# Optimization experiments

Measured on AMD Instinct MI355X. Metric: run time of the kernel, lower is better.

The kernel has to match this reference:

```python
import jax, jax.numpy as jnp
import numpy as np
import math

B, S, DIM = 2, 4096, 1024
H, HD = 16, 64            # n_heads, head_dim
BLK, TOPK = 512, 3        # moba_block_size, moba_topk
NEG_INF = -10000.0


def setup_inputs() -> dict:
    key = jax.random.key(0)
    ks = jax.random.split(key, 5)
    scale = 1.0 / math.sqrt(DIM)
    x = jax.random.normal(ks[0], (B, S, DIM), dtype=jnp.float32)
    wq = jax.random.normal(ks[1], (DIM, DIM), dtype=jnp.float32) * scale
    wk = jax.random.normal(ks[2], (DIM, DIM), dtype=jnp.float32) * scale
    wv = jax.random.normal(ks[3], (DIM, DIM), dtype=jnp.float32) * scale
    wo = jax.random.normal(ks[4], (DIM, DIM), dtype=jnp.float32) * scale
    # rotary tables over half of head_dim
    inv_freq = 1.0 / (10000.0 ** (jnp.arange(0, HD, 2, dtype=jnp.float32) / HD))
    ang = jnp.arange(S, dtype=jnp.float32)[:, None] * inv_freq[None, :]  # [S, HD//2]
    return {"x": x, "wq": wq, "wk": wk, "wv": wv, "wo": wo,
            "cos": jnp.cos(ang), "sin": jnp.sin(ang)}


def _rotate(t, cos, sin):
    # t: [B, H, S, HD]; rotate-half rotary embedding
    c = cos[None, None, :, :]
    s = sin[None, None, :, :]
    t1, t2 = jnp.split(t, 2, axis=-1)
    return jnp.concatenate([t1 * c - t2 * s, t1 * s + t2 * c], axis=-1)


def _moba_forward(x, wq, wk, wv, wo, cos, sin):
    bs, seq_len, dim = x.shape
    inv_sqrt_d = 1.0 / math.sqrt(HD)
    q = (x @ wq).reshape(bs, seq_len, H, HD).transpose(0, 2, 1, 3)  # [B,H,S,D]
    k = (x @ wk).reshape(bs, seq_len, H, HD).transpose(0, 2, 1, 3)
    v = (x @ wv).reshape(bs, seq_len, H, HD).transpose(0, 2, 1, 3)
    q = _rotate(q, cos, sin)
    k = _rotate(k, cos, sin)

    nb = seq_len // BLK  # num_blocks (S divisible by BLK -> pad_len = 0)
    k_blocks = k.reshape(bs, H, nb, BLK, HD)
    v_blocks = v.reshape(bs, H, nb, BLK, HD)

    # gating: q against block means, with block-causal mask
    block_repr = k_blocks.mean(axis=3)  # [B,H,nb,D]
    gating = jnp.einsum('bhsd,bhnd->bhsn', q, block_repr) * inv_sqrt_d
    q_block = jnp.arange(seq_len) // BLK
    future = q_block[:, None] < jnp.arange(nb)[None, :]  # [S, nb]
    gating = jnp.where(future[None, None], NEG_INF, gating)
    _, sel = jax.lax.top_k(gating, TOPK)  # [B,H,S,TOPK]

    # one chunk per block of queries; chunk uses indices of its middle query
    nc = seq_len // BLK
    mids = jnp.arange(nc) * BLK + BLK // 2
    chunk_sel = sel[:, :, mids, :]  # [B,H,nc,TOPK]

    idx = chunk_sel.reshape(bs, H, nc * TOPK)[..., None, None]  # [B,H,nc*k,1,1]
    k_sel = jnp.take_along_axis(k_blocks, idx, axis=2).reshape(bs, H, nc, TOPK * BLK, HD)
    v_sel = jnp.take_along_axis(v_blocks, idx, axis=2).reshape(bs, H, nc, TOPK * BLK, HD)

    q_ch = q.reshape(bs, H, nc, BLK, HD)
    scores = jnp.einsum('bhcqd,bhckd->bhcqk', q_ch, k_sel) * inv_sqrt_d
    probs = jax.nn.softmax(scores.astype(jnp.float32), axis=-1).astype(scores.dtype)
    out = jnp.einsum('bhcqk,bhckd->bhcqd', probs, v_sel)  # [B,H,nc,BLK,D]
    out = out.reshape(bs, H, seq_len, HD).transpose(0, 2, 1, 3).reshape(bs, seq_len, dim)
    return out @ wo


def reference(x, wq, wk, wv, wo, cos, sin):
    return _moba_forward(x, wq, wk, wv, wo, cos, sin)
```

## Files before the change

### kernel.cpp

```cpp
#include <hip/hip_runtime.h>

typedef short bf16x8 __attribute__((ext_vector_type(8)));
typedef float f32x4 __attribute__((ext_vector_type(4)));
typedef float f32x16 __attribute__((ext_vector_type(16)));

#define AS1 __attribute__((address_space(1)))
#define AS3 __attribute__((address_space(3)))
#define GLOAD16(g, l) __builtin_amdgcn_global_load_lds((const AS1 unsigned int*)(g), (AS3 unsigned int*)(l), 16, 0, 0)

#define B_   2
#define S_   4096
#define DIM_ 1024
#define H_   16
#define HD_  64
#define BLK_ 512
#define SCLQ 0.18033688011112042f

static __device__ __forceinline__ unsigned short f2bf(float x){
  unsigned int u = __builtin_bit_cast(unsigned int, x);
  u += 0x7fffu + ((u >> 16) & 1u);
  return (unsigned short)(u >> 16);
}

static __device__ __forceinline__ unsigned cvtpk(float lo, float hi){
  unsigned r;
  asm("v_cvt_pk_bf16_f32 %0, %1, %2" : "=v"(r) : "v"(lo), "v"(hi));
  return r;
}
static __device__ __forceinline__ void plswap(unsigned &a, unsigned &b){
  asm("v_permlane32_swap_b32 %0, %1" : "+v"(a), "+v"(b));
}
static __device__ __forceinline__ bf16x8 mkpa(unsigned a, unsigned b, unsigned c, unsigned d){
  int4 v = make_int4((int)a,(int)b,(int)c,(int)d);
  return __builtin_bit_cast(bf16x8, v);
}

__global__ __launch_bounds__(256) void k_convert_x(const float4* __restrict__ x, ushort4* __restrict__ xb){
  int i = blockIdx.x * 256 + threadIdx.x;
  float4 v = x[i];
  xb[i] = make_ushort4(f2bf(v.x), f2bf(v.y), f2bf(v.z), f2bf(v.w));
}

__global__ __launch_bounds__(256) void k_transpose_w(
    const float* __restrict__ w0, const float* __restrict__ w1,
    const float* __restrict__ w2, const float* __restrict__ w3,
    unsigned short* __restrict__ wqkvT, unsigned short* __restrict__ woT){
  __shared__ float tl[32][33];
  int z = blockIdx.z;
  const float* w = z==0 ? w0 : z==1 ? w1 : z==2 ? w2 : w3;
  unsigned short* t = (z==3) ? woT : (wqkvT + (size_t)z*1024*1024);
  int nb = blockIdx.x*32, kb = blockIdx.y*32;
  int tx = threadIdx.x & 31, ty = threadIdx.x >> 5;
  #pragma unroll
  for(int i=0;i<4;i++) tl[ty+8*i][tx] = w[(size_t)(kb+ty+8*i)*DIM_ + nb+tx];
  __syncthreads();
  #pragma unroll
  for(int i=0;i<4;i++) t[(size_t)(nb+ty+8*i)*DIM_ + kb+tx] = f2bf(tl[tx][ty+8*i]);
}

__global__ __launch_bounds__(256) void k_prepw(const float* __restrict__ cosT, const float* __restrict__ sinT,
                                               float* __restrict__ W){
  int idx = blockIdx.x*256 + threadIdx.x;
  int s = idx >> 6, j = idx & 63;
  W[idx] = (j < 32) ? cosT[s*32 + j] : sinT[s*32 + j - 32];
}

__global__ __launch_bounds__(256) void k_xp(const float* __restrict__ x, const float* __restrict__ W,
                                            float* __restrict__ Xp2){
  __shared__ float Xl[16*128];
  __shared__ float Wl[16*64];
  int bid = blockIdx.x;
  int dt = bid & 7, ss = (bid>>3)&1, n = (bid>>4)&7, b = bid>>7;
  int tid = threadIdx.x;
  int jt = tid & 15, dtl = tid >> 4;
  int dbase = dt*128;
  int s0 = n*512 + ss*256;
  f32x4 acc[8];
  #pragma unroll
  for(int i=0;i<8;i++) acc[i] = (f32x4){0.f,0.f,0.f,0.f};

  for(int ch=0; ch<16; ch++){
    int sb = s0 + ch*16;
    #pragma unroll
    for(int i=0;i<2;i++){
      int g = i*256 + tid;
      int row = g>>5, col = g&31;
      GLOAD16(x + ((size_t)b*S_ + sb + row)*DIM_ + dbase + col*4, (char*)Xl + g*16);
    }
    {
      int row = tid>>4, col = tid&15;
      GLOAD16(W + (size_t)(sb + row)*64 + col*4, (char*)Wl + tid*16);
    }
    __syncthreads();
    #pragma unroll
    for(int s=0;s<16;s++){
      f32x4 wv = *(const f32x4*)&Wl[s*64 + jt*4];
      f32x4 x0 = *(const f32x4*)&Xl[s*128 + dtl*8];
      f32x4 x1 = *(const f32x4*)&Xl[s*128 + dtl*8 + 4];
      #pragma unroll
      for(int dd=0;dd<4;dd++) acc[dd]   += wv * x0[dd];
      #pragma unroll
      for(int dd=0;dd<4;dd++) acc[dd+4] += wv * x1[dd];
    }
    __syncthreads();
  }
  size_t base = ((size_t)(ss*16 + b*8 + n))*1024;
  #pragma unroll
  for(int dd=0;dd<8;dd++){
    size_t row = base + dbase + dtl*8 + dd;
    *(f32x4*)&Xp2[row*64 + jt*4] = acc[dd];
  }
}

__global__ __launch_bounds__(256) void k_bsum(const float* __restrict__ Xp2, const float* __restrict__ wk,
                                              float* __restrict__ bsum){
  __shared__ float red[4][64];
  int bid = blockIdx.x;
  int h = bid & 15, n = (bid>>4)&7, b = bid>>7;
  int tid = threadIdx.x;
  int jj = tid & 63, dgrp = tid >> 6;
  int j = jj & 31;
  size_t r0 = ((size_t)(b*8 + n))*1024;
  size_t r1 = ((size_t)(16 + b*8 + n))*1024;
  float acc = 0.0f;
  for(int i=0;i<256;i++){
    int d = dgrp*256 + i;
    float xc = Xp2[(r0 + d)*64 + j]      + Xp2[(r1 + d)*64 + j];
    float xs = Xp2[(r0 + d)*64 + 32 + j] + Xp2[(r1 + d)*64 + 32 + j];
    float u = wk[(size_t)d*1024 + h*64 + j];
    float v = wk[(size_t)d*1024 + h*64 + 32 + j];
    acc += (jj < 32) ? (xc*u - xs*v) : (xs*u + xc*v);
  }
  red[dgrp][jj] = acc;
  __syncthreads();
  if(tid < 64){
    float s = red[0][tid] + red[1][tid] + red[2][tid] + red[3][tid];
    bsum[(((size_t)(b*16+h))*8 + n)*64 + tid] = s;
  }
}

__global__ __launch_bounds__(256) void k_qmid(const float* __restrict__ x, const float* __restrict__ wq,
                                              float* __restrict__ qpart){
  __shared__ float xr[128];
  int bid = blockIdx.x;
  int ks  = blockIdx.y;
  int b = bid >> 3, c = bid & 7;
  int mid = c*BLK_ + BLK_/2;
  int tid = threadIdx.x;
  if(tid < 128) xr[tid] = x[((size_t)b*S_ + mid)*DIM_ + ks*128 + tid];
  __syncthreads();
  float acc[4] = {0,0,0,0};
  for(int k=0;k<128;k++){
    float xv = xr[k];
    #pragma unroll
    for(int i=0;i<4;i++) acc[i] += xv * wq[(size_t)(ks*128+k)*1024 + i*256 + tid];
  }
  #pragma unroll
  for(int i=0;i<4;i++) qpart[((size_t)ks*16 + bid)*1024 + i*256 + tid] = acc[i];
}

__global__ __launch_bounds__(256) void k_sel(const float* __restrict__ qpart, const float* __restrict__ bsum,
                                             const float* __restrict__ cosT, const float* __restrict__ sinT,
                                             int* __restrict__ sel){
  int bid = blockIdx.x;
  int b = bid >> 3, c = bid & 7;
  int mid = c*BLK_ + BLK_/2;
  int tid = threadIdx.x;
  int hg = tid >> 4, ln = tid & 15;
  size_t qb0 = (size_t)bid*1024 + hg*64;
  auto qsum = [&](int idx){
    float s = 0.0f;
    #pragma unroll
    for(int ks=0;ks<8;ks++) s += qpart[(size_t)ks*16384 + qb0 + idx];
    return s;
  };
  float rv[4];
  #pragma unroll
  for(int i=0;i<4;i++){
    int jj = ln*4 + i; int j = jj & 31;
    float q1 = qsum(j), q2 = qsum(32+j);
    float c0 = cosT[(size_t)mid*32 + j], s0 = sinT[(size_t)mid*32 + j];
    rv[i] = (jj < 32) ? (q1*c0 - q2*s0) : (q1*s0 + q2*c0);
  }
  float g[8];
  #pragma unroll
  for(int n=0;n<8;n++){
    const float* bs = bsum + (((size_t)(b*16+hg))*8 + n)*64 + ln*4;
    float p = rv[0]*bs[0] + rv[1]*bs[1] + rv[2]*bs[2] + rv[3]*bs[3];
    p += __shfl_xor(p,1); p += __shfl_xor(p,2); p += __shfl_xor(p,4); p += __shfl_xor(p,8);
    g[n] = p * (1.0f/512.0f) * 0.125f;
  }
  if(ln == 0){
    for(int n=c+1;n<8;n++) g[n] = -10000.0f;
    int base = ((b*16+hg)*8 + c)*3;
    #pragma unroll
    for(int t=0;t<3;t++){
      int bi = 0; float bv = g[0];
      for(int n=1;n<8;n++) if(g[n] > bv){ bv = g[n]; bi = n; }
      sel[base + t] = bi;
      g[bi] = -3.4e38f;
    }
  }
}

template<int MODE>
__global__ __launch_bounds__(512, 2) void k_gemmq(const unsigned short* __restrict__ A,
                                                  const unsigned short* __restrict__ Bt,
                                                  unsigned short* __restrict__ dq, unsigned short* __restrict__ dk,
                                                  unsigned short* __restrict__ dv, float* __restrict__ dstf,
                                                  const float* __restrict__ cosT, const float* __restrict__ sinT,
                                                  int M, int N, int K){
  __shared__ unsigned short lA[2][128*64];
  __shared__ unsigned short lB[2][128*64];
  int bm = blockIdx.y*128, bn = blockIdx.x*128;
  int tid = threadIdx.x, w = tid>>6, lane = tid&63;
  int wr = w>>1, wc = w&1;
  int l15 = lane&15, lh = lane>>4;
  f32x4 acc[2][4];
  f32x4 zero = {0.f,0.f,0.f,0.f};
  #pragma unroll
  for(int m=0;m<2;m++)
    #pragma unroll
    for(int n=0;n<4;n++) acc[m][n] = zero;

  auto STAGE = [&](int bsel, int k0){
    #pragma unroll
    for(int i=0;i<2;i++){
      int g = i*512 + tid;
      int row = g>>3, slot = (g&7)^(row&7);
      GLOAD16(A  + (size_t)(bm+row)*K + k0 + slot*8, (char*)lA[bsel] + g*16);
      GLOAD16(Bt + (size_t)(bn+row)*K + k0 + slot*8, (char*)lB[bsel] + g*16);
    }
  };

  int NT = K >> 6;
  STAGE(0, 0);
  STAGE(1, 64);
  int cur = 0;

  for(int t=0;t<NT;t++){
    if(t < NT-1) asm volatile("s_waitcnt vmcnt(4)" ::: "memory");
    else         asm volatile("s_waitcnt vmcnt(0)" ::: "memory");
    asm volatile("s_barrier" ::: "memory");

    #pragma unroll
    for(int kk=0;kk<2;kk++){
      bf16x8 af[2], bfr[4];
      #pragma unroll
      for(int m=0;m<2;m++){
        int r = wr*32 + m*16 + l15;
        af[m] = *(const bf16x8*)((const char*)lA[cur] + r*128 + (((kk*4+lh)^(r&7))*16));
      }
      #pragma unroll
      for(int n=0;n<4;n++){
        int r = wc*64 + n*16 + l15;
        bfr[n] = *(const bf16x8*)((const char*)lB[cur] + r*128 + (((kk*4+lh)^(r&7))*16));
      }
      __builtin_amdgcn_s_setprio(1);
      #pragma unroll
      for(int m=0;m<2;m++)
        #pragma unroll
        for(int n=0;n<4;n++)
          acc[m][n] = __builtin_amdgcn_mfma_f32_16x16x32_bf16(af[m], bfr[n], acc[m][n], 0, 0, 0);
      __builtin_amdgcn_s_setprio(0);
    }

    asm volatile("s_barrier" ::: "memory");
    if(t+2 < NT) STAGE(cur, (t+2)*64);
    cur ^= 1;
  }

  if(MODE == 2){
    #pragma unroll
    for(int m=0;m<2;m++){
      int row0 = bm + wr*32 + m*16 + lh*4;
      #pragma unroll
      for(int n=0;n<4;n++){
        int col = bn + wc*64 + n*16 + l15;
        #pragma unroll
        for(int r=0;r<4;r++) dstf[(size_t)(row0+r)*N + col] = acc[m][n][r];
      }
    }
  } else {
    int sec = bn >> 10;
    int nloc = (bn & 1023) + wc*64;
    if(sec == 2){
      #pragma unroll
      for(int m=0;m<2;m++){
        int s0 = bm + wr*32 + m*16 + lh*4;
        int bb = s0 >> 12, sl = s0 & 4095;
        #pragma unroll
        for(int n=0;n<4;n++){
          int d = nloc + n*16 + l15;
          ushort4 pk = make_ushort4(f2bf(acc[m][n][0]), f2bf(acc[m][n][1]),
                                    f2bf(acc[m][n][2]), f2bf(acc[m][n][3]));
          *(ushort4*)&dv[((size_t)(bb*1024 + d))*4096 + sl] = pk;
        }
      }
    } else {
      unsigned short* dst = (sec == 0) ? dq : dk;
      float scl = (sec == 0) ? SCLQ : 1.0f;
      int h = nloc >> 6;
      #pragma unroll
      for(int m=0;m<2;m++){
        int row0 = bm + wr*32 + m*16 + lh*4;
        #pragma unroll
        for(int n=0;n<2;n++){
          int f = n*16 + l15;
          #pragma unroll
          for(int r=0;r<4;r++){
            int row = row0 + r;
            int bb = row >> 12, s = row & 4095;
            float c0 = cosT[(size_t)s*32 + f]*scl, s0 = sinT[(size_t)s*32 + f]*scl;
            float a1 = acc[m][n][r], a2 = acc[m][n+2][r];
            size_t base = ((size_t)(bb*16 + h)*4096 + s)*64;
            dst[base + f]      = f2bf(a1*c0 - a2*s0);
            dst[base + 32 + f] = f2bf(a1*s0 + a2*c0);
          }
        }
      }
    }
  }
}

__global__ __launch_bounds__(256, 4) void k_attn(const unsigned short* __restrict__ q,
                                                 const unsigned short* __restrict__ kb,
                                                 const unsigned short* __restrict__ vt,
                                                 const int* __restrict__ sel,
                                                 unsigned short* __restrict__ attnb){
  __shared__ unsigned short lK[2][64*64];
  __shared__ unsigned short lV[2][64*64];
  int cbh = blockIdx.x, qt = blockIdx.y;
  int bh = cbh >> 3, c = cbh & 7;
  int b = bh >> 4, h = bh & 15;
  int tid = threadIdx.x, w = tid>>6, lane = tid&63;
  int ql = lane&31, hi = lane>>5;
  int q0 = c*BLK_ + qt*128 + w*32;

  const int* selp = sel + (bh*8 + c)*3;
  int sb0 = selp[0], sb1 = selp[1], sb2 = selp[2];

  int r0 = tid>>3, sl = (tid&7) ^ (r0&7);
  const unsigned short* kbase = kb + ((size_t)bh*S_ + r0)*64 + (size_t)sl*8;
  const unsigned short* vbase = vt + ((size_t)(b*1024 + h*64 + r0))*S_ + (size_t)sl*8;

  bf16x8 qf[4];
  #pragma unroll
  for(int kk=0;kk<4;kk++)
    qf[kk] = *(const bf16x8*)(q + ((size_t)bh*S_ + q0 + ql)*64 + kk*16 + hi*8);

  f32x16 o[2], o2;
  f32x16 zero16 = {0,0,0,0,0,0,0,0,0,0,0,0,0,0,0,0};
  o[0] = zero16; o[1] = zero16; o2 = zero16;
  short one_bf = (short)0x3F80;
  bf16x8 ones = {one_bf,one_bf,one_bf,one_bf,one_bf,one_bf,one_bf,one_bf};

  auto STAGE = [&](int bsel, int t){
    int seg = t>>3;
    int blk = seg==0 ? sb0 : (seg==1 ? sb1 : sb2);
    int soff = blk*BLK_ + (t&7)*64;
    #pragma unroll
    for(int i=0;i<2;i++){
      GLOAD16(kbase + (size_t)(soff + i*32)*64, (char*)lK[bsel] + (i*256 + w*64)*16);
      GLOAD16(vbase + (size_t)i*32*S_ + soff,   (char*)lV[bsel] + (i*256 + w*64)*16);
    }
  };

  STAGE(0, 0);
  __syncthreads();
  int cur = 0;

  for(int t=0;t<24;t++){
    if(t+1 < 24) STAGE(cur^1, t+1);

    f32x16 sc[2];
    sc[0] = zero16; sc[1] = zero16;
    __builtin_amdgcn_s_setprio(1);
    #pragma unroll
    for(int g=0;g<2;g++){
      int key = g*32 + ql;
      #pragma unroll
      for(int kk=0;kk<4;kk++){
        bf16x8 kf = *(const bf16x8*)((const char*)lK[cur] + key*128 + ((kk*32 + hi*16) ^ ((ql&7)<<4)));
        sc[g] = __builtin_amdgcn_mfma_f32_32x32x16_bf16(kf, qf[kk], sc[g], 0, 0, 0);
      }
    }
    __builtin_amdgcn_s_setprio(0);

    #pragma unroll
    for(int r=0;r<16;r++){
      sc[0][r] = exp2f(sc[0][r]);
      sc[1][r] = exp2f(sc[1][r]);
    }

    __builtin_amdgcn_s_setprio(1);
    #pragma unroll
    for(int g=0;g<2;g++){
      unsigned u0 = cvtpk(sc[g][0],  sc[g][1]);
      unsigned u1 = cvtpk(sc[g][4],  sc[g][5]);
      plswap(u0, u1);
      unsigned u2 = cvtpk(sc[g][2],  sc[g][3]);
      unsigned u3 = cvtpk(sc[g][6],  sc[g][7]);
      plswap(u2, u3);
      unsigned u4 = cvtpk(sc[g][8],  sc[g][9]);
      unsigned u5 = cvtpk(sc[g][12], sc[g][13]);
      plswap(u4, u5);
      unsigned u6 = cvtpk(sc[g][10], sc[g][11]);
      unsigned u7 = cvtpk(sc[g][14], sc[g][15]);
      plswap(u6, u7);
      bf16x8 pa0 = mkpa(u0,u2,u1,u3);
      bf16x8 pa1 = mkpa(u4,u6,u5,u7);
      #pragma unroll
      for(int dh=0;dh<2;dh++){
        int d = dh*32 + ql;
        bf16x8 v0 = *(const bf16x8*)((const char*)lV[cur] + d*128 + ((g*64 + hi*16) ^ ((d&7)<<4)));
        o[dh] = __builtin_amdgcn_mfma_f32_32x32x16_bf16(pa0, v0, o[dh], 0, 0, 0);
        bf16x8 v1 = *(const bf16x8*)((const char*)lV[cur] + d*128 + ((g*64 + 32 + hi*16) ^ ((d&7)<<4)));
        o[dh] = __builtin_amdgcn_mfma_f32_32x32x16_bf16(pa1, v1, o[dh], 0, 0, 0);
      }
      o2 = __builtin_amdgcn_mfma_f32_32x32x16_bf16(pa0, ones, o2, 0, 0, 0);
      o2 = __builtin_amdgcn_mfma_f32_32x32x16_bf16(pa1, ones, o2, 0, 0, 0);
    }
    __builtin_amdgcn_s_setprio(0);

    __syncthreads();
    cur ^= 1;
  }

  #pragma unroll
  for(int r=0;r<16;r++){
    float inv = 1.0f / o2[r];
    int cr = (r&3) + 8*(r>>2) + 4*hi;
    int s = q0 + cr;
    size_t base = ((size_t)(b*S_ + s))*1024 + h*64;
    attnb[base + ql]      = f2bf(o[0][r]*inv);
    attnb[base + 32 + ql] = f2bf(o[1][r]*inv);
  }
}

extern "C" void kernel_launch(void* const* d_in, const int* in_sizes, int n_in,
                              void* d_out, int out_size, void* d_ws, size_t ws_size,
                              hipStream_t stream){
  const float* x    = (const float*)d_in[0];
  const float* wq   = (const float*)d_in[1];
  const float* wk   = (const float*)d_in[2];
  const float* wv   = (const float*)d_in[3];
  const float* wo   = (const float*)d_in[4];
  const float* cosT = (const float*)d_in[5];
  const float* sinT = (const float*)d_in[6];

  char* p = (char*)d_ws;
  unsigned short* xbf   = (unsigned short*)p; p += (size_t)8192*1024*2;
  unsigned short* wqkvT = (unsigned short*)p; p += (size_t)3072*1024*2;
  unsigned short* woT   = (unsigned short*)p; p += (size_t)1024*1024*2;
  unsigned short* qb  = (unsigned short*)p; p += (size_t)8192*1024*2;
  unsigned short* kbf = (unsigned short*)p; p += (size_t)8192*1024*2;
  unsigned short* vtb = (unsigned short*)p; p += (size_t)8192*1024*2;
  float* Wsel = (float*)p; p += (size_t)4096*64*4;
  float* Xp2  = (float*)p; p += (size_t)2*16*1024*64*4;
  float* bsum = (float*)p; p += (size_t)2*16*8*64*4;
  float* qmid = (float*)p; p += (size_t)16*1024*4;
  int*   sel  = (int*)p;   p += (size_t)2*16*8*3*4;
  unsigned short* attnb = xbf;
  float* qpart = Wsel;
  if((size_t)(p - (char*)d_ws) > ws_size) return;

  k_convert_x<<<8192, 256, 0, stream>>>((const float4*)x, (ushort4*)xbf);
  k_transpose_w<<<dim3(32,32,4), 256, 0, stream>>>(wq,wk,wv,wo, wqkvT, woT);
  k_prepw<<<1024, 256, 0, stream>>>(cosT, sinT, Wsel);
  k_xp<<<256, 256, 0, stream>>>(x, Wsel, Xp2);
  k_bsum<<<256, 256, 0, stream>>>(Xp2, wk, bsum);
  k_qmid<<<dim3(16,8), 256, 0, stream>>>(x, wq, qpart);
  k_sel<<<16, 256, 0, stream>>>(qpart, bsum, cosT, sinT, sel);
  k_gemmq<0><<<dim3(24,64), 512, 0, stream>>>(xbf, wqkvT, qb, kbf, vtb, nullptr, cosT, sinT, 8192, 3072, 1024);
  k_attn<<<dim3(256,4), 256, 0, stream>>>(qb, kbf, vtb, sel, attnb);
  k_gemmq<2><<<dim3(8,64), 512, 0, stream>>>(attnb, woT, nullptr, nullptr, nullptr, (float*)d_out, nullptr, nullptr, 8192, 1024, 1024);
}
```

Before: 265.7 us.

## Fuse preprocessing kernels into one launch with block-range dispatch

Merges the x conversion, weight transpose, rotary-projected x accumulation and mid-query projection kernels into a single kernel that dispatches on block index ranges. It also drops the separate cos/sin table packing kernel by loading cos and sin directly in the Xp stage. This removes several launch gaps and lets the independent small jobs overlap on the GPU. The trade-off is higher shared memory use per block, since all branches' buffers are allocated, which may lower occupancy for the simple conversion blocks.

```diff
diff --git a/kernel.cpp b/kernel.cpp
--- a/kernel.cpp
+++ b/kernel.cpp
@@ -35,80 +35,93 @@
   return __builtin_bit_cast(bf16x8, v);
 }
 
-__global__ __launch_bounds__(256) void k_convert_x(const float4* __restrict__ x, ushort4* __restrict__ xb){
-  int i = blockIdx.x * 256 + threadIdx.x;
-  float4 v = x[i];
-  xb[i] = make_ushort4(f2bf(v.x), f2bf(v.y), f2bf(v.z), f2bf(v.w));
-}
-
-__global__ __launch_bounds__(256) void k_transpose_w(
-    const float* __restrict__ w0, const float* __restrict__ w1,
-    const float* __restrict__ w2, const float* __restrict__ w3,
-    unsigned short* __restrict__ wqkvT, unsigned short* __restrict__ woT){
+__global__ __launch_bounds__(256) void k_pre(const float* __restrict__ x,
+                                             const float* __restrict__ w0, const float* __restrict__ w1,
+                                             const float* __restrict__ w2, const float* __restrict__ w3,
+                                             const float* __restrict__ cosT, const float* __restrict__ sinT,
+                                             ushort4* __restrict__ xb,
+                                             unsigned short* __restrict__ wqkvT, unsigned short* __restrict__ woT,
+                                             float* __restrict__ Xp2, float* __restrict__ qpart){
   __shared__ float tl[32][33];
-  int z = blockIdx.z;
-  const float* w = z==0 ? w0 : z==1 ? w1 : z==2 ? w2 : w3;
-  unsigned short* t = (z==3) ? woT : (wqkvT + (size_t)z*1024*1024);
-  int nb = blockIdx.x*32, kb = blockIdx.y*32;
-  int tx = threadIdx.x & 31, ty = threadIdx.x >> 5;
-  #pragma unroll
-  for(int i=0;i<4;i++) tl[ty+8*i][tx] = w[(size_t)(kb+ty+8*i)*DIM_ + nb+tx];
-  __syncthreads();
-  #pragma unroll
-  for(int i=0;i<4;i++) t[(size_t)(nb+ty+8*i)*DIM_ + kb+tx] = f2bf(tl[tx][ty+8*i]);
-}
-
-__global__ __launch_bounds__(256) void k_prepw(const float* __restrict__ cosT, const float* __restrict__ sinT,
-                                               float* __restrict__ W){
-  int idx = blockIdx.x*256 + threadIdx.x;
-  int s = idx >> 6, j = idx & 63;
-  W[idx] = (j < 32) ? cosT[s*32 + j] : sinT[s*32 + j - 32];
-}
-
-__global__ __launch_bounds__(256) void k_xp(const float* __restrict__ x, const float* __restrict__ W,
-                                            float* __restrict__ Xp2){
   __shared__ float Xl[16*128];
   __shared__ float Wl[16*64];
-  int bid = blockIdx.x;
-  int dt = bid & 7, ss = (bid>>3)&1, n = (bid>>4)&7, b = bid>>7;
-  int tid = threadIdx.x;
-  int jt = tid & 15, dtl = tid >> 4;
-  int dbase = dt*128;
-  int s0 = n*512 + ss*256;
-  f32x4 acc[8];
-  #pragma unroll
-  for(int i=0;i<8;i++) acc[i] = (f32x4){0.f,0.f,0.f,0.f};
-
-  for(int ch=0; ch<16; ch++){
-    int sb = s0 + ch*16;
-    #pragma unroll
-    for(int i=0;i<2;i++){
-      int g = i*256 + tid;
-      int row = g>>5, col = g&31;
-      GLOAD16(x + ((size_t)b*S_ + sb + row)*DIM_ + dbase + col*4, (char*)Xl + g*16);
-    }
-    {
-      int row = tid>>4, col = tid&15;
-      GLOAD16(W + (size_t)(sb + row)*64 + col*4, (char*)Wl + tid*16);
-    }
+  __shared__ float xr[128];
+  int bid = blockIdx.x, tid = threadIdx.x;
+
+  if(bid < 8192){
+    int i = bid*256 + tid;
+    float4 v = ((const float4*)x)[i];
+    xb[i] = make_ushort4(f2bf(v.x), f2bf(v.y), f2bf(v.z), f2bf(v.w));
+  } else if(bid < 12288){
+    int zi = bid - 8192;
+    int z = zi >> 10, rem = zi & 1023;
+    const float* w = z==0 ? w0 : z==1 ? w1 : z==2 ? w2 : w3;
+    unsigned short* t = (z==3) ? woT : (wqkvT + (size_t)z*1024*1024);
+    int nb = (rem & 31)*32, kb = (rem >> 5)*32;
+    int tx = tid & 31, ty = tid >> 5;
+    #pragma unroll
+    for(int i=0;i<4;i++) tl[ty+8*i][tx] = w[(size_t)(kb+ty+8*i)*DIM_ + nb+tx];
     __syncthreads();
     #pragma unroll
-    for(int s=0;s<16;s++){
-      f32x4 wv = *(const f32x4*)&Wl[s*64 + jt*4];
-      f32x4 x0 = *(const f32x4*)&Xl[s*128 + dtl*8];
-      f32x4 x1 = *(const f32x4*)&Xl[s*128 + dtl*8 + 4];
-      #pragma unroll
-      for(int dd=0;dd<4;dd++) acc[dd]   += wv * x0[dd];
-      #pragma unroll
-      for(int dd=0;dd<4;dd++) acc[dd+4] += wv * x1[dd];
-    }
+    for(int i=0;i<4;i++) t[(size_t)(nb+ty+8*i)*DIM_ + kb+tx] = f2bf(tl[tx][ty+8*i]);
+  } else if(bid < 12544){
+    int bid2 = bid - 12288;
+    int dt = bid2 & 7, ss = (bid2>>3)&1, n = (bid2>>4)&7, b = bid2>>7;
+    int jt = tid & 15, dtl = tid >> 4;
+    int dbase = dt*128;
+    int s0 = n*512 + ss*256;
+    f32x4 acc[8];
+    #pragma unroll
+    for(int i=0;i<8;i++) acc[i] = (f32x4){0.f,0.f,0.f,0.f};
+
+    for(int ch=0; ch<16; ch++){
+      int sb = s0 + ch*16;
+      #pragma unroll
+      for(int i=0;i<2;i++){
+        int g = i*256 + tid;
+        int row = g>>5, col = g&31;
+        GLOAD16(x + ((size_t)b*S_ + sb + row)*DIM_ + dbase + col*4, (char*)Xl + g*16);
+      }
+      {
+        int row = tid>>4, col = tid&15;
+        const float* src = (col < 8) ? (cosT + (size_t)(sb + row)*32 + col*4)
+                                     : (sinT + (size_t)(sb + row)*32 + (col-8)*4);
+        GLOAD16(src, (char*)Wl + tid*16);
+      }
+      __syncthreads();
+      #pragma unroll
+      for(int s=0;s<16;s++){
+        f32x4 wv = *(const f32x4*)&Wl[s*64 + jt*4];
+        f32x4 x0 = *(const f32x4*)&Xl[s*128 + dtl*8];
+        f32x4 x1 = *(const f32x4*)&Xl[s*128 + dtl*8 + 4];
+        #pragma unroll
+        for(int dd=0;dd<4;dd++) acc[dd]   += wv * x0[dd];
+        #pragma unroll
+        for(int dd=0;dd<4;dd++) acc[dd+4] += wv * x1[dd];
+      }
+      __syncthreads();
+    }
+    size_t base = ((size_t)(ss*16 + b*8 + n))*1024;
+    #pragma unroll
+    for(int dd=0;dd<8;dd++){
+      size_t row = base + dbase + dtl*8 + dd;
+      *(f32x4*)&Xp2[row*64 + jt*4] = acc[dd];
+    }
+  } else {
+    int bid3 = bid - 12544;
+    int bidq = bid3 & 15, ks = bid3 >> 4;
+    int b = bidq >> 3, c = bidq & 7;
+    int mid = c*BLK_ + BLK_/2;
+    if(tid < 128) xr[tid] = x[((size_t)b*S_ + mid)*DIM_ + ks*128 + tid];
     __syncthreads();
-  }
-  size_t base = ((size_t)(ss*16 + b*8 + n))*1024;
-  #pragma unroll
-  for(int dd=0;dd<8;dd++){
-    size_t row = base + dbase + dtl*8 + dd;
-    *(f32x4*)&Xp2[row*64 + jt*4] = acc[dd];
+    float acc[4] = {0,0,0,0};
+    for(int k=0;k<128;k++){
+      float xv = xr[k];
+      #pragma unroll
+      for(int i=0;i<4;i++) acc[i] += xv * w0[(size_t)(ks*128+k)*1024 + i*256 + tid];
+    }
+    #pragma unroll
+    for(int i=0;i<4;i++) qpart[((size_t)ks*16 + bidq)*1024 + i*256 + tid] = acc[i];
   }
 }
 
@@ -139,26 +152,6 @@
   }
 }
 
-__global__ __launch_bounds__(256) void k_qmid(const float* __restrict__ x, const float* __restrict__ wq,
-                                              float* __restrict__ qpart){
-  __shared__ float xr[128];
-  int bid = blockIdx.x;
-  int ks  = blockIdx.y;
-  int b = bid >> 3, c = bid & 7;
-  int mid = c*BLK_ + BLK_/2;
-  int tid = threadIdx.x;
-  if(tid < 128) xr[tid] = x[((size_t)b*S_ + mid)*DIM_ + ks*128 + tid];
-  __syncthreads();
-  float acc[4] = {0,0,0,0};
-  for(int k=0;k<128;k++){
-    float xv = xr[k];
-    #pragma unroll
-    for(int i=0;i<4;i++) acc[i] += xv * wq[(size_t)(ks*128+k)*1024 + i*256 + tid];
-  }
-  #pragma unroll
-  for(int i=0;i<4;i++) qpart[((size_t)ks*16 + bid)*1024 + i*256 + tid] = acc[i];
-}
-
 __global__ __launch_bounds__(256) void k_sel(const float* __restrict__ qpart, const float* __restrict__ bsum,
                                              const float* __restrict__ cosT, const float* __restrict__ sinT,
                                              int* __restrict__ sel){
@@ -465,12 +458,9 @@
   float* qpart = Wsel;
   if((size_t)(p - (char*)d_ws) > ws_size) return;
 
-  k_convert_x<<<8192, 256, 0, stream>>>((const float4*)x, (ushort4*)xbf);
-  k_transpose_w<<<dim3(32,32,4), 256, 0, stream>>>(wq,wk,wv,wo, wqkvT, woT);
-  k_prepw<<<1024, 256, 0, stream>>>(cosT, sinT, Wsel);
-  k_xp<<<256, 256, 0, stream>>>(x, Wsel, Xp2);
+  k_pre<<<12672, 256, 0, stream>>>(x, wq, wk, wv, wo, cosT, sinT,
+                                   (ushort4*)xbf, wqkvT, woT, Xp2, qpart);
   k_bsum<<<256, 256, 0, stream>>>(Xp2, wk, bsum);
-  k_qmid<<<dim3(16,8), 256, 0, stream>>>(x, wq, qpart);
   k_sel<<<16, 256, 0, stream>>>(qpart, bsum, cosT, sinT, sel);
   k_gemmq<0><<<dim3(24,64), 512, 0, stream>>>(xbf, wqkvT, qb, kbf, vtb, nullptr, cosT, sinT, 8192, 3072, 1024);
   k_attn<<<dim3(256,4), 256, 0, stream>>>(qb, kbf, vtb, sel, attnb);
```

Measured after the change: 274.2 us. +3.2%, slower.
